# Kernel optimization log

Hardware: AMD Instinct MI355X
Metric: run time of the kernel (lower is better)

Reference implementation:

```python
import jax, jax.numpy as jnp
import numpy as np

G = 8           # graphs
NBG = 1024      # blocks per graph
APB = 4         # atoms per block
NC = 1          # coord channels
HID = 512
ES = 64
K = 9
L = 3
NLVL = 50
NB = G * NBG
NU = NB * APB
NUM_BLOCK, NUM_ATOM, NUM_POS = 25, 16, 16
BIG = 1e9


def _cumsum_ids(seg_lengths, n):
    # faithful to torch: zeros, mark segment starts via cumsum(lengths)[:-1], cumsum
    ids = jnp.zeros((n,), jnp.int32).at[jnp.cumsum(seg_lengths)[:-1]].set(1)
    return jnp.cumsum(ids)


def setup_inputs() -> dict:
    key = jax.random.key(0)
    ks = jax.random.split(key, 18)
    s = 0.02
    return {
        'Z': 3.0 * jax.random.normal(ks[0], (NU, NC, 3), jnp.float32),
        'B': jax.random.randint(ks[1], (NB,), 0, NUM_BLOCK),
        'A': jax.random.randint(ks[2], (NU,), 0, NUM_ATOM),
        'atom_positions': jax.random.randint(ks[3], (NU,), 0, NUM_POS),
        'block_lengths': jnp.full((NB,), APB, jnp.int32),
        'lengths': jnp.full((G,), NBG, jnp.int32),
        'segment_ids': jax.random.randint(ks[4], (NB,), 0, 2),
        'noise': jax.random.normal(ks[5], (NU, NC, 3), jnp.float32),
        'noise_level': jax.random.randint(ks[6], (G,), 0, NLVL),
        'sigmas': jnp.asarray(np.exp(np.linspace(np.log(10.0), np.log(0.01), NLVL)), jnp.float32),
        'atom_emb': s * jax.random.normal(ks[7], (NUM_ATOM, HID), jnp.float32),
        'pos_emb': s * jax.random.normal(ks[8], (NUM_POS, HID), jnp.float32),
        'block_emb': s * jax.random.normal(ks[9], (NUM_BLOCK, HID), jnp.float32),
        'edge_emb': s * jax.random.normal(ks[10], (2, ES), jnp.float32),
        'Wm': s * jax.random.normal(ks[11], (L, HID, HID), jnp.float32),
        'We': s * jax.random.normal(ks[12], (L, ES, HID), jnp.float32),
        'Wu': s * jax.random.normal(ks[13], (L, HID, HID), jnp.float32),
        'wz': s * jax.random.normal(ks[14], (L, HID), jnp.float32),
        'W1': s * jax.random.normal(ks[15], (HID, HID), jnp.float32),
        'b1': jnp.zeros((HID,), jnp.float32),
        'W2': s * jax.random.normal(ks[16], (HID, 1), jnp.float32),
    }


def _forward(Z, B, A, atom_positions, block_lengths, lengths, segment_ids,
             noise, noise_level, sigmas, atom_emb, pos_emb, block_emb, edge_emb,
             Wm, We, Wu, wz, W1, b1, W2):
    nb, nu, g = B.shape[0], A.shape[0], lengths.shape[0]
    nbg, apb = nb // g, nu // nb
    batch_id = _cumsum_ids(lengths, nb)        # [Nb]
    block_id = _cumsum_ids(block_lengths, nu)  # [Nu]

    # perturb: Z + noise * sigma[noise_level[graph]]
    used = sigmas[noise_level][batch_id][block_id]          # [Nu]
    Zp = Z + noise * used[:, None, None]                    # [Nu, NC, 3]

    # block embedding: atom + position + block-type
    H0 = atom_emb[A] + pos_emb[atom_positions] + block_emb[B][block_id]  # [Nu, H]

    # edges: fully connect -> split intra/inter by segment -> knn by min atom-pair distance
    xa = Zp.reshape(g, nbg * apb * NC, 3)
    sq = jnp.sum(xa * xa, axis=-1)
    d2 = sq[:, :, None] + sq[:, None, :] - 2.0 * jnp.einsum('gnd,gmd->gnm', xa, xa)
    D = d2.reshape(g, nbg, apb * NC, nbg, apb * NC).min(axis=(2, 4))     # [g, nbg, nbg]
    seg = segment_ids.reshape(g, nbg)
    same = seg[:, :, None] == seg[:, None, :]
    eye = jnp.eye(nbg, dtype=bool)[None]
    _, idx_intra = jax.lax.top_k(-jnp.where(same & ~eye, D, BIG), K)     # [g, nbg, K]
    _, idx_inter = jax.lax.top_k(-jnp.where(~same, D, BIG), K)
    off = (jnp.arange(g, dtype=jnp.int32) * nbg)[:, None, None]
    dst_loc = jnp.broadcast_to(jnp.arange(nbg, dtype=jnp.int32)[None, :, None] + off, (g, nbg, K))
    src = jnp.concatenate([(idx_intra + off).reshape(-1), (idx_inter + off).reshape(-1)])
    dst = jnp.concatenate([dst_loc.reshape(-1), dst_loc.reshape(-1)])
    eattr = edge_emb[jnp.concatenate([jnp.zeros(g * nbg * K, jnp.int32), jnp.ones(g * nbg * K, jnp.int32)])]

    # encoder (GET surrogate): block-level equivariant message passing
    h = jax.ops.segment_sum(H0, block_id, num_segments=nb) / apb                    # [Nb, H]
    Zb0 = jax.ops.segment_sum(Zp.mean(axis=1), block_id, num_segments=nb) / apb    # [Nb, 3]
    Zb = Zb0
    for l in range(Wm.shape[0]):
        m = jax.nn.silu((h[src] + h[dst]) @ Wm[l] + eattr @ We[l])                  # [E, H]
        h = h + jax.nn.silu(jax.ops.segment_sum(m, dst, num_segments=nb) @ Wu[l])
        coef = jnp.tanh(m @ wz[l])                                                  # [E]
        Zb = Zb + jax.ops.segment_sum((Zb[src] - Zb[dst]) * coef[:, None], dst, num_segments=nb) / (2 * K)
    pred_Z = Zp + (Zb - Zb0)[block_id][:, None, :]
    unit_repr = H0 + h[block_id]
    block_repr = h
    graph_repr = jax.ops.segment_sum(h, batch_id, num_segments=g)

    # energy head: SiLU -> Linear -> SiLU -> Linear(no bias), summed per graph
    e = jax.nn.silu(jax.nn.silu(block_repr) @ W1 + b1) @ W2                         # [Nb, 1]
    pred_energy = jax.ops.segment_sum(e[:, 0], batch_id, num_segments=g)            # [g]

    pred_noise = pred_Z - Zp
    per_unit = jnp.sum((pred_noise - noise) ** 2, axis=(-1, -2))                    # [Nu]
    nl = jax.ops.segment_sum(per_unit, batch_id[block_id], num_segments=g)
    loss = 0.5 * nl.mean()
    return pred_energy, pred_noise, unit_repr, block_repr, graph_repr, loss


def reference(Z, B, A, atom_positions, block_lengths, lengths, segment_ids,
              noise, noise_level, sigmas, atom_emb, pos_emb, block_emb, edge_emb,
              Wm, We, Wu, wz, W1, b1, W2):
    return _forward(Z, B, A, atom_positions, block_lengths, lengths, segment_ids,
                    noise, noise_level, sigmas, atom_emb, pos_emb, block_emb, edge_emb,
                    Wm, We, Wu, wz, W1, b1, W2)
```

## Files before the change

### kernel.cpp

```cpp
#include <hip/hip_runtime.h>
#include <hip/hip_bf16.h>

typedef __bf16 bf16;
typedef __bf16 bf16x2 __attribute__((ext_vector_type(2)));
typedef __bf16 bf16x8 __attribute__((ext_vector_type(8)));
typedef float floatx4 __attribute__((ext_vector_type(4)));

#define NB_ 8192
#define NU_ 32768

__device__ __forceinline__ float silu_f(float x) {
    float e = __expf(-x);
    return x * __builtin_amdgcn_rcpf(1.0f + e);
}

__global__ void transpose_weights(const float* __restrict__ Wm, const float* __restrict__ Wu,
                                  const float* __restrict__ W1,
                                  bf16* __restrict__ WmT, bf16* __restrict__ WuT, bf16* __restrict__ W1T) {
    int z = blockIdx.z;
    const float* src; bf16* dst;
    if (z < 3)      { src = Wm + (size_t)z*262144;     dst = WmT + (size_t)z*262144; }
    else if (z < 6) { src = Wu + (size_t)(z-3)*262144; dst = WuT + (size_t)(z-3)*262144; }
    else            { src = W1;                        dst = W1T; }
    __shared__ float tile[32][33];
    int tx = threadIdx.x, ty = threadIdx.y;
    int x = blockIdx.x*32 + tx;
    int y0 = blockIdx.y*32;
    #pragma unroll
    for (int i = 0; i < 32; i += 8)
        tile[ty+i][tx] = src[(size_t)(y0+ty+i)*512 + x];
    __syncthreads();
    int xo = blockIdx.y*32 + tx;
    int yo0 = blockIdx.x*32;
    #pragma unroll
    for (int i = 0; i < 32; i += 8)
        dst[(size_t)(yo0+ty+i)*512 + xo] = (bf16)tile[tx][ty+i];
}

__global__ void ebias_kernel(const float* __restrict__ edge_emb, const float* __restrict__ We,
                             float* __restrict__ ebias) {
    int gid = blockIdx.x*256 + threadIdx.x;
    if (gid >= 3072) return;
    int l = gid >> 10, t = (gid >> 9) & 1, c = gid & 511;
    float s = 0.0f;
    #pragma unroll 8
    for (int e = 0; e < 64; e++)
        s += edge_emb[t*64 + e] * We[(size_t)(l*64 + e)*512 + c];
    ebias[gid] = s;
}

__global__ void setup_kernel(const float* __restrict__ Z, const float* __restrict__ noise,
                             const int* __restrict__ noise_level, const float* __restrict__ sigmas,
                             const int* __restrict__ Aarr, const int* __restrict__ posa,
                             const int* __restrict__ Barr,
                             const float* __restrict__ atom_emb, const float* __restrict__ pos_emb,
                             const float* __restrict__ block_emb,
                             float* __restrict__ Zp, float* __restrict__ Zb0, float* __restrict__ Zb,
                             float* __restrict__ hf, bf16* __restrict__ hb) {
    int b = blockIdx.x;
    int tid = threadIdx.x;
    int g = b >> 10;
    __shared__ float zsh[12];
    if (tid < 12) {
        float sig = sigmas[noise_level[g]];
        int idx = b*12 + tid;
        float zp = Z[idx] + noise[idx]*sig;
        Zp[idx] = zp;
        zsh[tid] = zp;
    }
    __syncthreads();
    if (tid < 3) {
        float v = 0.25f*(zsh[tid] + zsh[3+tid] + zsh[6+tid] + zsh[9+tid]);
        Zb0[b*3+tid] = v; Zb[b*3+tid] = v;
    }
    int ai[4], pi[4];
    #pragma unroll
    for (int a = 0; a < 4; a++) { ai[a] = Aarr[b*4+a]*512; pi[a] = posa[b*4+a]*512; }
    int bb = Barr[b]*512;
    for (int c = tid; c < 512; c += 128) {
        float s = 0.0f;
        #pragma unroll
        for (int a = 0; a < 4; a++) s += atom_emb[ai[a]+c] + pos_emb[pi[a]+c];
        s = 0.25f*s + block_emb[bb+c];
        hf[(size_t)b*512+c] = s;
        hb[(size_t)b*512+c] = (bf16)s;
    }
}

__global__ __launch_bounds__(256) void knn_kernel(const float* __restrict__ Zp,
                                                  const int* __restrict__ seg,
                                                  int* __restrict__ nbr) {
    int wid = threadIdx.x >> 6;
    int lane = threadIdx.x & 63;
    int r = blockIdx.x*4 + wid;
    int g = r >> 10;
    int il = r & 1023;
    int segr = seg[r];
    float za[4][3];
    #pragma unroll
    for (int a = 0; a < 4; a++)
        #pragma unroll
        for (int d = 0; d < 3; d++)
            za[a][d] = Zp[r*12 + a*3 + d];
    float dist[16];
    unsigned smask = 0;
    int base = g << 10;
    #pragma unroll
    for (int t = 0; t < 16; t++) {
        int j = t*64 + lane;
        int jb = base + j;
        const float4* p = (const float4*)(Zp + (size_t)jb*12);
        float4 v0 = p[0], v1 = p[1], v2 = p[2];
        float bx[4] = {v0.x, v0.w, v1.z, v2.y};
        float by[4] = {v0.y, v1.x, v1.w, v2.z};
        float bz[4] = {v0.z, v1.y, v2.x, v2.w};
        float dm = 3.0e38f;
        #pragma unroll
        for (int a = 0; a < 4; a++) {
            #pragma unroll
            for (int bq = 0; bq < 4; bq++) {
                float dx = za[a][0]-bx[bq], dy = za[a][1]-by[bq], dz = za[a][2]-bz[bq];
                float dd = dx*dx + dy*dy + dz*dz;
                dm = fminf(dm, dd);
            }
        }
        dist[t] = dm;
        if (seg[jb] == segr) smask |= (1u << t);
    }
    unsigned removed = 0;
    for (int phase = 0; phase < 2; phase++) {
        for (int it = 0; it < 9; it++) {
            float bestd = 3.0e38f; int bestt = 0;
            #pragma unroll
            for (int t = 0; t < 16; t++) {
                int j = t*64 + lane;
                bool ok = (phase == 0) ? (((smask>>t)&1u) && (j != il))
                                       : (!((smask>>t)&1u));
                ok = ok && !((removed>>t)&1u);
                float dv = ok ? dist[t] : 1.0e9f;
                if (dv < bestd) { bestd = dv; bestt = t; }
            }
            int bestj = bestt*64 + lane;
            unsigned long long key =
                (((unsigned long long)__float_as_uint(bestd)) << 32) | (unsigned)bestj;
            #pragma unroll
            for (int off = 32; off >= 1; off >>= 1) {
                unsigned long long o = __shfl_xor(key, off, 64);
                if (o < key) key = o;
            }
            int jwin = (int)(key & 0xffffffffu);
            if (lane == 0) nbr[r*18 + phase*9 + it] = base + jwin;
            if ((jwin & 63) == lane) removed |= (1u << (jwin >> 6));
        }
    }
}

__global__ __launch_bounds__(256) void gemm_kernel(const bf16* __restrict__ A, const bf16* __restrict__ BT,
                                                   float* __restrict__ C, float* __restrict__ hf,
                                                   bf16* __restrict__ hb, bf16* __restrict__ shp,
                                                   const float* __restrict__ b1,
                                                   const float* __restrict__ W2,
                                                   float* __restrict__ eblk,
                                                   int mode) {
    int bid = blockIdx.x;
    int mt = bid & 63, nt = bid >> 6;
    int m0 = mt*128, n0 = nt*64;
    int tid = threadIdx.x, lane = tid & 63, wid = tid >> 6;
    int wm = wid & 1, wn = wid >> 1;
    int lm = lane & 15, q = lane >> 4;
    __shared__ alignas(16) bf16 sA[128*40];
    __shared__ alignas(16) bf16 sB[64*40];
    floatx4 zv = {0.0f, 0.0f, 0.0f, 0.0f};
    floatx4 acc[4][2];
    #pragma unroll
    for (int i = 0; i < 4; i++)
        #pragma unroll
        for (int j = 0; j < 2; j++) acc[i][j] = zv;
    for (int k0 = 0; k0 < 512; k0 += 32) {
        #pragma unroll
        for (int it = 0; it < 2; it++) {
            int idx = tid + it*256;
            int row = idx >> 2, qt = idx & 3;
            *(int4*)(sA + row*40 + qt*8) = *(const int4*)(A + (size_t)(m0+row)*512 + k0 + qt*8);
        }
        {
            int row = tid >> 2, qt = tid & 3;
            *(int4*)(sB + row*40 + qt*8) = *(const int4*)(BT + (size_t)(n0+row)*512 + k0 + qt*8);
        }
        __syncthreads();
        bf16x8 af[4], bfr[2];
        #pragma unroll
        for (int tm = 0; tm < 4; tm++)
            af[tm] = *(const bf16x8*)(sA + (wm*64 + tm*16 + lm)*40 + q*8);
        #pragma unroll
        for (int tn = 0; tn < 2; tn++)
            bfr[tn] = *(const bf16x8*)(sB + (wn*32 + tn*16 + lm)*40 + q*8);
        #pragma unroll
        for (int tm = 0; tm < 4; tm++)
            #pragma unroll
            for (int tn = 0; tn < 2; tn++)
                acc[tm][tn] = __builtin_amdgcn_mfma_f32_16x16x32_bf16(af[tm], bfr[tn], acc[tm][tn], 0, 0, 0);
        __syncthreads();
    }
    if (mode == 2) {
        #pragma unroll
        for (int tm = 0; tm < 4; tm++) {
            #pragma unroll
            for (int rr = 0; rr < 4; rr++) {
                float part = 0.0f;
                #pragma unroll
                for (int tn = 0; tn < 2; tn++) {
                    int col = n0 + wn*32 + tn*16 + lm;
                    float t = silu_f(acc[tm][tn][rr] + b1[col]);
                    part += t * W2[col];
                }
                part += __shfl_xor(part, 1, 64);
                part += __shfl_xor(part, 2, 64);
                part += __shfl_xor(part, 4, 64);
                part += __shfl_xor(part, 8, 64);
                if (lm == 0) {
                    int row = m0 + wm*64 + tm*16 + q*4 + rr;
                    atomicAdd(&eblk[row], part);
                }
            }
        }
        return;
    }
    #pragma unroll
    for (int tm = 0; tm < 4; tm++) {
        #pragma unroll
        for (int tn = 0; tn < 2; tn++) {
            #pragma unroll
            for (int rr = 0; rr < 4; rr++) {
                int row = m0 + wm*64 + tm*16 + q*4 + rr;
                int col = n0 + wn*32 + tn*16 + lm;
                size_t o = (size_t)row*512 + col;
                float v = acc[tm][tn][rr];
                if (mode == 0) {
                    C[o] = v;
                } else {
                    float nh = hf[o] + silu_f(v);
                    hf[o] = nh;
                    hb[o] = (bf16)nh;
                    if (shp) shp[o] = (bf16)silu_f(nh);
                }
            }
        }
    }
}

__global__ __launch_bounds__(256) void edge_kernel(const float* __restrict__ P, const float* __restrict__ ebias,
                                                   const float* __restrict__ wz, const float* __restrict__ Zb,
                                                   const int* __restrict__ nbr, bf16* __restrict__ msum,
                                                   float* __restrict__ zacc) {
    int b = blockIdx.x, tid = threadIdx.x;
    int c0 = 2*tid;
    int lane = tid & 63, wid = tid >> 6;
    __shared__ int srcs[18];
    __shared__ float red[18][4];
    __shared__ float term[18][3];
    if (tid < 18) srcs[tid] = nbr[b*18 + tid];
    __syncthreads();
    float2 pd  = *(const float2*)(P + (size_t)b*512 + c0);
    float2 eb0 = *(const float2*)(ebias + c0);
    float2 eb1 = *(const float2*)(ebias + 512 + c0);
    float2 w   = *(const float2*)(wz + c0);
    float ms0 = 0.0f, ms1 = 0.0f;
    float pdot[18];
    #pragma unroll
    for (int e = 0; e < 18; e++) {
        int s = srcs[e];
        float2 pv = *(const float2*)(P + (size_t)s*512 + c0);
        float ba = (e < 9) ? eb0.x : eb1.x;
        float bb = (e < 9) ? eb0.y : eb1.y;
        float m0 = silu_f(pv.x + pd.x + ba);
        float m1 = silu_f(pv.y + pd.y + bb);
        ms0 += m0; ms1 += m1;
        pdot[e] = m0*w.x + m1*w.y;
    }
    bf16x2 mp = { (bf16)ms0, (bf16)ms1 };
    *(bf16x2*)(msum + (size_t)b*512 + c0) = mp;
    #pragma unroll
    for (int e = 0; e < 18; e++) {
        float v = pdot[e];
        #pragma unroll
        for (int off = 32; off >= 1; off >>= 1) v += __shfl_xor(v, off, 64);
        if (lane == 0) red[e][wid] = v;
    }
    __syncthreads();
    if (tid < 18) {
        float dot = red[tid][0] + red[tid][1] + red[tid][2] + red[tid][3];
        float coef = tanhf(dot);
        int s = srcs[tid];
        #pragma unroll
        for (int d = 0; d < 3; d++)
            term[tid][d] = (Zb[s*3 + d] - Zb[b*3 + d]) * coef;
    }
    __syncthreads();
    if (tid < 3) {
        float s = 0.0f;
        #pragma unroll
        for (int e = 0; e < 18; e++) s += term[e][tid];
        zacc[b*3 + tid] = s;
    }
}

__global__ void zb_apply(float* __restrict__ Zb, const float* __restrict__ zacc) {
    int i = blockIdx.x*256 + threadIdx.x;
    if (i < NB_*3) Zb[i] += zacc[i] * (1.0f/18.0f);
}

__global__ void energy_kernel(const float* __restrict__ eblk, float* __restrict__ out_e) {
    int g = blockIdx.x, tid = threadIdx.x;
    __shared__ float red[256];
    float s = 0.0f;
    #pragma unroll
    for (int k = 0; k < 4; k++) s += eblk[g*1024 + k*256 + tid];
    red[tid] = s; __syncthreads();
    for (int st = 128; st > 0; st >>= 1) {
        if (tid < st) red[tid] += red[tid+st];
        __syncthreads();
    }
    if (tid == 0) out_e[g] = red[0];
}

__global__ void graphrepr_kernel(const float* __restrict__ h, float* __restrict__ out_gr) {
    int g = blockIdx.x >> 5;
    int rc = (blockIdx.x >> 1) & 15;
    int ch = blockIdx.x & 1;
    int c = ch*256 + threadIdx.x;
    int b0 = (g << 10) + rc*64;
    float s = 0.0f;
    for (int i = 0; i < 64; i++) s += h[(size_t)(b0+i)*512 + c];
    atomicAdd(&out_gr[g*512 + c], s);
}

__global__ void prednoise_loss_kernel(const float* __restrict__ Zb, const float* __restrict__ Zb0,
                                      const float* __restrict__ noise,
                                      float* __restrict__ out_pn, float* __restrict__ out_loss) {
    int u = blockIdx.x*256 + threadIdx.x;
    int b = u >> 2;
    float per = 0.0f;
    #pragma unroll
    for (int d = 0; d < 3; d++) {
        float dv = Zb[b*3+d] - Zb0[b*3+d];
        out_pn[u*3+d] = dv;
        float e = dv - noise[u*3+d];
        per += e*e;
    }
    __shared__ float red[256];
    red[threadIdx.x] = per; __syncthreads();
    for (int st = 128; st > 0; st >>= 1) {
        if (threadIdx.x < st) red[threadIdx.x] += red[threadIdx.x+st];
        __syncthreads();
    }
    if (threadIdx.x == 0) atomicAdd(out_loss, red[0] * (1.0f/16.0f));
}

__global__ void unitrepr_kernel(const int* __restrict__ Aarr, const int* __restrict__ posa,
                                const int* __restrict__ Barr,
                                const float* __restrict__ atom_emb, const float* __restrict__ pos_emb,
                                const float* __restrict__ block_emb,
                                const float* __restrict__ h, float* __restrict__ out_ur) {
    #pragma unroll
    for (int k = 0; k < 4; k++) {
        int idx = blockIdx.x*1024 + k*256 + threadIdx.x;
        int u = idx >> 9, c = idx & 511, b = u >> 2;
        out_ur[idx] = atom_emb[Aarr[u]*512+c] + pos_emb[posa[u]*512+c]
                    + block_emb[Barr[b]*512+c] + h[(size_t)b*512+c];
    }
}

extern "C" void kernel_launch(void* const* d_in, const int* in_sizes, int n_in,
                              void* d_out, int out_size, void* d_ws, size_t ws_size,
                              hipStream_t stream) {
    const float* Z         = (const float*)d_in[0];
    const int*   B         = (const int*)d_in[1];
    const int*   A         = (const int*)d_in[2];
    const int*   ap        = (const int*)d_in[3];
    const int*   seg       = (const int*)d_in[6];
    const float* noise     = (const float*)d_in[7];
    const int*   nl        = (const int*)d_in[8];
    const float* sig       = (const float*)d_in[9];
    const float* atom_emb  = (const float*)d_in[10];
    const float* pos_emb   = (const float*)d_in[11];
    const float* block_emb = (const float*)d_in[12];
    const float* edge_emb  = (const float*)d_in[13];
    const float* Wm        = (const float*)d_in[14];
    const float* We        = (const float*)d_in[15];
    const float* Wu        = (const float*)d_in[16];
    const float* wz        = (const float*)d_in[17];
    const float* W1        = (const float*)d_in[18];
    const float* b1        = (const float*)d_in[19];
    const float* W2        = (const float*)d_in[20];
    (void)in_sizes; (void)n_in; (void)d_ws; (void)ws_size; (void)out_size;

    float* out = (float*)d_out;
    const size_t o1 = 8, o2 = 98312, o3 = 16875528, o4 = 21069832, o5 = 21073928;
    float* out_e    = out;
    float* out_pn   = out + o1;
    float* out_ur   = out + o2;
    float* hf       = out + o3;
    float* out_gr   = out + o4;
    float* out_loss = out + o5;

    char* arena = (char*)(out + o2);
    float* P    = (float*)(arena);
    bf16*  msum = (bf16*)(arena + 16777216);
    bf16*  sh   = (bf16*)(arena + 25165824);
    bf16*  hb   = (bf16*)(arena + 33554432);
    float* Zp   = (float*)(arena + 41943040);
    float* Zb0  = (float*)(arena + 42336256);
    float* Zb   = (float*)(arena + 42434560);
    float* zacc = (float*)(arena + 42532864);
    int*   nbr  = (int*)  (arena + 42631168);
    bf16*  WmT  = (bf16*) (arena + 43220992);
    bf16*  WuT  = (bf16*) (arena + 44793856);
    bf16*  W1T  = (bf16*) (arena + 46366720);
    float* ebias= (float*)(arena + 46891008);
    float* eblk = (float*)(arena + 46903296);

    hipMemsetAsync(out_loss, 0, 4, stream);
    hipMemsetAsync(out_gr, 0, 8*512*4, stream);
    hipMemsetAsync(eblk, 0, NB_*4, stream);
    transpose_weights<<<dim3(16,16,7), dim3(32,8), 0, stream>>>(Wm, Wu, W1, WmT, WuT, W1T);
    ebias_kernel<<<12, 256, 0, stream>>>(edge_emb, We, ebias);
    setup_kernel<<<8192, 128, 0, stream>>>(Z, noise, nl, sig, A, ap, B,
                                           atom_emb, pos_emb, block_emb,
                                           Zp, Zb0, Zb, hf, hb);
    knn_kernel<<<2048, 256, 0, stream>>>(Zp, seg, nbr);
    for (int l = 0; l < 3; l++) {
        gemm_kernel<<<512, 256, 0, stream>>>(hb, WmT + (size_t)l*262144, P,
                                             nullptr, nullptr, nullptr, nullptr, nullptr, nullptr, 0);
        edge_kernel<<<8192, 256, 0, stream>>>(P, ebias + l*1024, wz + l*512, Zb, nbr, msum, zacc);
        gemm_kernel<<<512, 256, 0, stream>>>(msum, WuT + (size_t)l*262144, nullptr,
                                             hf, hb, (l == 2) ? sh : nullptr, nullptr, nullptr, nullptr, 1);
        zb_apply<<<96, 256, 0, stream>>>(Zb, zacc);
    }
    gemm_kernel<<<512, 256, 0, stream>>>(sh, W1T, nullptr, nullptr, nullptr, nullptr,
                                         b1, W2, eblk, 2);
    energy_kernel<<<8, 256, 0, stream>>>(eblk, out_e);
    graphrepr_kernel<<<256, 256, 0, stream>>>(hf, out_gr);
    prednoise_loss_kernel<<<128, 256, 0, stream>>>(Zb, Zb0, noise, out_pn, out_loss);
    unitrepr_kernel<<<16384, 256, 0, stream>>>(A, ap, B, atom_emb, pos_emb, block_emb, hf, out_ur);
}
```

Before: 528.9 us.

## Fuse setup kernels, overlap KNN with first GEMM, use bf16 P and LDS-direct loads

The init kernels (setup, weight transpose, ebias, memsets) are merged into one launch, and the KNN search is merged with the first message GEMM so the two run concurrently. zb_apply is folded into the update GEMM, and the energy, graph-repr and loss kernels are merged into one finalize kernel. The GEMM now uses global_load_lds with an XOR-swizzled LDS layout, the P intermediate is stored as bf16 to halve its traffic, KNN selection uses a float min-reduce plus ballot, and unitrepr is vectorised with float4. Risks: storing P in bf16 lowers precision, and the zb update inside the GEMM must not race with the edge kernel that reads Zb.

```diff
diff --git a/kernel.cpp b/kernel.cpp
--- a/kernel.cpp
+++ b/kernel.cpp
@@ -14,87 +14,109 @@
     return x * __builtin_amdgcn_rcpf(1.0f + e);
 }
 
-__global__ void transpose_weights(const float* __restrict__ Wm, const float* __restrict__ Wu,
-                                  const float* __restrict__ W1,
-                                  bf16* __restrict__ WmT, bf16* __restrict__ WuT, bf16* __restrict__ W1T) {
-    int z = blockIdx.z;
-    const float* src; bf16* dst;
-    if (z < 3)      { src = Wm + (size_t)z*262144;     dst = WmT + (size_t)z*262144; }
-    else if (z < 6) { src = Wu + (size_t)(z-3)*262144; dst = WuT + (size_t)(z-3)*262144; }
-    else            { src = W1;                        dst = W1T; }
+__device__ __forceinline__ float2 unpack_bf2(unsigned v) {
+    float2 r;
+    r.x = __uint_as_float(v << 16);
+    r.y = __uint_as_float(v & 0xFFFF0000u);
+    return r;
+}
+
+__device__ __forceinline__ void gll16(const bf16* g, bf16* l) {
+    __builtin_amdgcn_global_load_lds((const __attribute__((address_space(1))) void*)g,
+                                     (__attribute__((address_space(3))) void*)l, 16, 0, 0);
+}
+
+__global__ __launch_bounds__(256) void init_kernel(
+    const float* __restrict__ Z, const float* __restrict__ noise,
+    const int* __restrict__ nl, const float* __restrict__ sig,
+    const int* __restrict__ Aarr, const int* __restrict__ posa, const int* __restrict__ Barr,
+    const float* __restrict__ atom_emb, const float* __restrict__ pos_emb,
+    const float* __restrict__ block_emb,
+    const float* __restrict__ edge_emb, const float* __restrict__ We,
+    const float* __restrict__ Wm, const float* __restrict__ Wu, const float* __restrict__ W1,
+    float* __restrict__ Zp, float* __restrict__ Zb0, float* __restrict__ Zb,
+    float* __restrict__ hf, bf16* __restrict__ hb,
+    bf16* __restrict__ WmT, bf16* __restrict__ WuT, bf16* __restrict__ W1T,
+    float* __restrict__ ebias,
+    float* __restrict__ out_gr, float* __restrict__ eblk, float* __restrict__ out_loss)
+{
+    __shared__ float zsh[12];
     __shared__ float tile[32][33];
-    int tx = threadIdx.x, ty = threadIdx.y;
-    int x = blockIdx.x*32 + tx;
-    int y0 = blockIdx.y*32;
-    #pragma unroll
-    for (int i = 0; i < 32; i += 8)
-        tile[ty+i][tx] = src[(size_t)(y0+ty+i)*512 + x];
-    __syncthreads();
-    int xo = blockIdx.y*32 + tx;
-    int yo0 = blockIdx.x*32;
-    #pragma unroll
-    for (int i = 0; i < 32; i += 8)
-        dst[(size_t)(yo0+ty+i)*512 + xo] = (bf16)tile[tx][ty+i];
-}
-
-__global__ void ebias_kernel(const float* __restrict__ edge_emb, const float* __restrict__ We,
-                             float* __restrict__ ebias) {
-    int gid = blockIdx.x*256 + threadIdx.x;
-    if (gid >= 3072) return;
-    int l = gid >> 10, t = (gid >> 9) & 1, c = gid & 511;
-    float s = 0.0f;
-    #pragma unroll 8
-    for (int e = 0; e < 64; e++)
-        s += edge_emb[t*64 + e] * We[(size_t)(l*64 + e)*512 + c];
-    ebias[gid] = s;
-}
-
-__global__ void setup_kernel(const float* __restrict__ Z, const float* __restrict__ noise,
-                             const int* __restrict__ noise_level, const float* __restrict__ sigmas,
-                             const int* __restrict__ Aarr, const int* __restrict__ posa,
-                             const int* __restrict__ Barr,
-                             const float* __restrict__ atom_emb, const float* __restrict__ pos_emb,
-                             const float* __restrict__ block_emb,
-                             float* __restrict__ Zp, float* __restrict__ Zb0, float* __restrict__ Zb,
-                             float* __restrict__ hf, bf16* __restrict__ hb) {
-    int b = blockIdx.x;
-    int tid = threadIdx.x;
-    int g = b >> 10;
-    __shared__ float zsh[12];
-    if (tid < 12) {
-        float sig = sigmas[noise_level[g]];
-        int idx = b*12 + tid;
-        float zp = Z[idx] + noise[idx]*sig;
-        Zp[idx] = zp;
-        zsh[tid] = zp;
-    }
-    __syncthreads();
-    if (tid < 3) {
-        float v = 0.25f*(zsh[tid] + zsh[3+tid] + zsh[6+tid] + zsh[9+tid]);
-        Zb0[b*3+tid] = v; Zb[b*3+tid] = v;
-    }
-    int ai[4], pi[4];
-    #pragma unroll
-    for (int a = 0; a < 4; a++) { ai[a] = Aarr[b*4+a]*512; pi[a] = posa[b*4+a]*512; }
-    int bb = Barr[b]*512;
-    for (int c = tid; c < 512; c += 128) {
+    int bid = blockIdx.x, tid = threadIdx.x;
+    if (bid < 8192) {
+        int b = bid, g = b >> 10;
+        if (tid < 12) {
+            float sg = sig[nl[g]];
+            int idx = b*12 + tid;
+            float zp = Z[idx] + noise[idx]*sg;
+            Zp[idx] = zp;
+            zsh[tid] = zp;
+        }
+        __syncthreads();
+        if (tid < 3) {
+            float v = 0.25f*(zsh[tid] + zsh[3+tid] + zsh[6+tid] + zsh[9+tid]);
+            Zb0[b*3+tid] = v; Zb[b*3+tid] = v;
+        }
+        int ai[4], pi[4];
+        #pragma unroll
+        for (int a = 0; a < 4; a++) { ai[a] = Aarr[b*4+a]*512; pi[a] = posa[b*4+a]*512; }
+        int bb = Barr[b]*512;
+        #pragma unroll
+        for (int cc = 0; cc < 2; cc++) {
+            int c = tid + cc*256;
+            float s = 0.0f;
+            #pragma unroll
+            for (int a = 0; a < 4; a++) s += atom_emb[ai[a]+c] + pos_emb[pi[a]+c];
+            s = 0.25f*s + block_emb[bb+c];
+            hf[(size_t)b*512+c] = s;
+            hb[(size_t)b*512+c] = (bf16)s;
+        }
+        return;
+    }
+    bid -= 8192;
+    if (bid < 1792) {
+        int z = bid >> 8, rem = bid & 255;
+        int bx = rem & 15, by = rem >> 4;
+        int tx = tid & 31, ty = tid >> 5;
+        const float* src; bf16* dst;
+        if (z < 3)      { src = Wm + (size_t)z*262144;     dst = WmT + (size_t)z*262144; }
+        else if (z < 6) { src = Wu + (size_t)(z-3)*262144; dst = WuT + (size_t)(z-3)*262144; }
+        else            { src = W1;                        dst = W1T; }
+        #pragma unroll
+        for (int i = 0; i < 32; i += 8)
+            tile[ty+i][tx] = src[(size_t)(by*32+ty+i)*512 + bx*32+tx];
+        __syncthreads();
+        #pragma unroll
+        for (int i = 0; i < 32; i += 8)
+            dst[(size_t)(bx*32+ty+i)*512 + by*32+tx] = (bf16)tile[tx][ty+i];
+        return;
+    }
+    bid -= 1792;
+    if (bid < 12) {
+        int gid = bid*256 + tid;
+        int l = gid >> 10, t = (gid >> 9) & 1, c = gid & 511;
         float s = 0.0f;
-        #pragma unroll
-        for (int a = 0; a < 4; a++) s += atom_emb[ai[a]+c] + pos_emb[pi[a]+c];
-        s = 0.25f*s + block_emb[bb+c];
-        hf[(size_t)b*512+c] = s;
-        hb[(size_t)b*512+c] = (bf16)s;
-    }
-}
-
-__global__ __launch_bounds__(256) void knn_kernel(const float* __restrict__ Zp,
-                                                  const int* __restrict__ seg,
-                                                  int* __restrict__ nbr) {
+        #pragma unroll 8
+        for (int e = 0; e < 64; e++)
+            s += edge_emb[t*64 + e] * We[(size_t)(l*64 + e)*512 + c];
+        ebias[gid] = s;
+        return;
+    }
+    bid -= 12;
+    int k = bid*256 + tid;
+    if (k < 4096) out_gr[k] = 0.0f;
+    else if (k < 12288) eblk[k-4096] = 0.0f;
+    else if (k == 12288) out_loss[0] = 0.0f;
+}
+
+__device__ void knn_body(int kb, const float* __restrict__ Zp, const int* __restrict__ seg,
+                         int* __restrict__ nbr) {
     int wid = threadIdx.x >> 6;
     int lane = threadIdx.x & 63;
-    int r = blockIdx.x*4 + wid;
+    int r = ((kb & 7) << 10) + ((kb >> 3) << 2) + wid;
     int g = r >> 10;
     int il = r & 1023;
+    int base = g << 10;
     int segr = seg[r];
     float za[4][3];
     #pragma unroll
@@ -104,11 +126,9 @@
             za[a][d] = Zp[r*12 + a*3 + d];
     float dist[16];
     unsigned smask = 0;
-    int base = g << 10;
     #pragma unroll
     for (int t = 0; t < 16; t++) {
-        int j = t*64 + lane;
-        int jb = base + j;
+        int jb = base + t*64 + lane;
         const float4* p = (const float4*)(Zp + (size_t)jb*12);
         float4 v0 = p[0], v1 = p[1], v2 = p[2];
         float bx[4] = {v0.x, v0.w, v1.z, v2.y};
@@ -120,81 +140,90 @@
             #pragma unroll
             for (int bq = 0; bq < 4; bq++) {
                 float dx = za[a][0]-bx[bq], dy = za[a][1]-by[bq], dz = za[a][2]-bz[bq];
-                float dd = dx*dx + dy*dy + dz*dz;
-                dm = fminf(dm, dd);
+                dm = fminf(dm, dx*dx + dy*dy + dz*dz);
             }
         }
         dist[t] = dm;
         if (seg[jb] == segr) smask |= (1u << t);
     }
-    unsigned removed = 0;
+    const float INF = 3.0e38f;
     for (int phase = 0; phase < 2; phase++) {
+        float wd[16];
+        #pragma unroll
+        for (int t = 0; t < 16; t++) {
+            bool ok = (phase == 0) ? (((smask >> t) & 1u) && (t*64 + lane != il))
+                                   : (!((smask >> t) & 1u));
+            wd[t] = ok ? dist[t] : INF;
+        }
         for (int it = 0; it < 9; it++) {
-            float bestd = 3.0e38f; int bestt = 0;
-            #pragma unroll
-            for (int t = 0; t < 16; t++) {
-                int j = t*64 + lane;
-                bool ok = (phase == 0) ? (((smask>>t)&1u) && (j != il))
-                                       : (!((smask>>t)&1u));
-                ok = ok && !((removed>>t)&1u);
-                float dv = ok ? dist[t] : 1.0e9f;
-                if (dv < bestd) { bestd = dv; bestt = t; }
-            }
-            int bestj = bestt*64 + lane;
-            unsigned long long key =
-                (((unsigned long long)__float_as_uint(bestd)) << 32) | (unsigned)bestj;
-            #pragma unroll
-            for (int off = 32; off >= 1; off >>= 1) {
-                unsigned long long o = __shfl_xor(key, off, 64);
-                if (o < key) key = o;
-            }
-            int jwin = (int)(key & 0xffffffffu);
-            if (lane == 0) nbr[r*18 + phase*9 + it] = base + jwin;
-            if ((jwin & 63) == lane) removed |= (1u << (jwin >> 6));
-        }
-    }
-}
-
-__global__ __launch_bounds__(256) void gemm_kernel(const bf16* __restrict__ A, const bf16* __restrict__ BT,
-                                                   float* __restrict__ C, float* __restrict__ hf,
-                                                   bf16* __restrict__ hb, bf16* __restrict__ shp,
-                                                   const float* __restrict__ b1,
-                                                   const float* __restrict__ W2,
-                                                   float* __restrict__ eblk,
-                                                   int mode) {
-    int bid = blockIdx.x;
+            float bd = wd[0]; int bt = 0;
+            #pragma unroll
+            for (int t = 1; t < 16; t++) { if (wd[t] < bd) { bd = wd[t]; bt = t; } }
+            float mv = bd;
+            #pragma unroll
+            for (int off = 32; off >= 1; off >>= 1) mv = fminf(mv, __shfl_xor(mv, off, 64));
+            unsigned long long msk = __ballot(bd == mv);
+            int wl = __ffsll(msk) - 1;
+            int wt = __shfl(bt, wl, 64);
+            if (lane == 0) nbr[r*18 + phase*9 + it] = base + wt*64 + wl;
+            bool amwin = (lane == wl);
+            #pragma unroll
+            for (int t = 0; t < 16; t++) if (amwin && t == wt) wd[t] = INF;
+        }
+    }
+}
+
+__device__ void gemm_body(const bf16* __restrict__ A, const bf16* __restrict__ BT,
+                          bf16* __restrict__ Pb, float* __restrict__ hf,
+                          bf16* __restrict__ hb, bf16* __restrict__ shp,
+                          const float* __restrict__ b1, const float* __restrict__ W2,
+                          float* __restrict__ eblk,
+                          float* __restrict__ Zb, const float* __restrict__ zacc,
+                          int mode, int bid)
+{
+    __shared__ alignas(16) bf16 sA[128*32];
+    __shared__ alignas(16) bf16 sB[64*32];
     int mt = bid & 63, nt = bid >> 6;
     int m0 = mt*128, n0 = nt*64;
-    int tid = threadIdx.x, lane = tid & 63, wid = tid >> 6;
-    int wm = wid & 1, wn = wid >> 1;
+    int tid = threadIdx.x, lane = tid & 63, w = tid >> 6;
+    int wm = w & 1, wn = w >> 1;
     int lm = lane & 15, q = lane >> 4;
-    __shared__ alignas(16) bf16 sA[128*40];
-    __shared__ alignas(16) bf16 sB[64*40];
+
+    int pA0 = w*128 + lane, pA1 = pA0 + 64, pB = w*64 + lane;
+    int rA0 = pA0 >> 2, qA0 = (pA0 & 3) ^ ((rA0 >> 1) & 3);
+    int rA1 = pA1 >> 2, qA1 = (pA1 & 3) ^ ((rA1 >> 1) & 3);
+    int rB  = pB  >> 2, qB  = (pB  & 3) ^ ((rB  >> 1) & 3);
+    const bf16* gA0 = A  + (size_t)(m0 + rA0)*512 + qA0*8;
+    const bf16* gA1 = A  + (size_t)(m0 + rA1)*512 + qA1*8;
+    const bf16* gB  = BT + (size_t)(n0 + rB )*512 + qB*8;
+    bf16* lA0 = sA + (w*128)*8;
+    bf16* lA1 = sA + (w*128 + 64)*8;
+    bf16* lB  = sB + (w*64)*8;
+
+    int swq = (q ^ ((lm >> 1) & 3)) * 8;
+    const bf16* pa[4]; const bf16* pb2[2];
+    #pragma unroll
+    for (int tm = 0; tm < 4; tm++) pa[tm] = sA + (wm*64 + tm*16 + lm)*32 + swq;
+    #pragma unroll
+    for (int tn = 0; tn < 2; tn++) pb2[tn] = sB + (wn*32 + tn*16 + lm)*32 + swq;
+
     floatx4 zv = {0.0f, 0.0f, 0.0f, 0.0f};
     floatx4 acc[4][2];
     #pragma unroll
     for (int i = 0; i < 4; i++)
         #pragma unroll
         for (int j = 0; j < 2; j++) acc[i][j] = zv;
+
     for (int k0 = 0; k0 < 512; k0 += 32) {
-        #pragma unroll
-        for (int it = 0; it < 2; it++) {
-            int idx = tid + it*256;
-            int row = idx >> 2, qt = idx & 3;
-            *(int4*)(sA + row*40 + qt*8) = *(const int4*)(A + (size_t)(m0+row)*512 + k0 + qt*8);
-        }
-        {
-            int row = tid >> 2, qt = tid & 3;
-            *(int4*)(sB + row*40 + qt*8) = *(const int4*)(BT + (size_t)(n0+row)*512 + k0 + qt*8);
-        }
+        gll16(gA0 + k0, lA0);
+        gll16(gA1 + k0, lA1);
+        gll16(gB  + k0, lB);
         __syncthreads();
         bf16x8 af[4], bfr[2];
         #pragma unroll
-        for (int tm = 0; tm < 4; tm++)
-            af[tm] = *(const bf16x8*)(sA + (wm*64 + tm*16 + lm)*40 + q*8);
-        #pragma unroll
-        for (int tn = 0; tn < 2; tn++)
-            bfr[tn] = *(const bf16x8*)(sB + (wn*32 + tn*16 + lm)*40 + q*8);
+        for (int tm = 0; tm < 4; tm++) af[tm] = *(const bf16x8*)pa[tm];
+        #pragma unroll
+        for (int tn = 0; tn < 2; tn++) bfr[tn] = *(const bf16x8*)pb2[tn];
         #pragma unroll
         for (int tm = 0; tm < 4; tm++)
             #pragma unroll
@@ -202,6 +231,16 @@
                 acc[tm][tn] = __builtin_amdgcn_mfma_f32_16x16x32_bf16(af[tm], bfr[tn], acc[tm][tn], 0, 0, 0);
         __syncthreads();
     }
+
+    if (mode == 1 && nt == 0) {
+        int o = m0*3 + tid;
+        Zb[o] += zacc[o] * (1.0f/18.0f);
+        if (tid < 128) {
+            int o2 = m0*3 + 256 + tid;
+            Zb[o2] += zacc[o2] * (1.0f/18.0f);
+        }
+    }
+
     if (mode == 2) {
         #pragma unroll
         for (int tm = 0; tm < 4; tm++) {
@@ -237,7 +276,7 @@
                 size_t o = (size_t)row*512 + col;
                 float v = acc[tm][tn][rr];
                 if (mode == 0) {
-                    C[o] = v;
+                    Pb[o] = (bf16)v;
                 } else {
                     float nh = hf[o] + silu_f(v);
                     hf[o] = nh;
@@ -249,11 +288,35 @@
     }
 }
 
-__global__ __launch_bounds__(256) void edge_kernel(const float* __restrict__ P, const float* __restrict__ ebias,
+__global__ __launch_bounds__(256) void gemm_kernel(const bf16* __restrict__ A, const bf16* __restrict__ BT,
+                                                   bf16* __restrict__ Pb, float* __restrict__ hf,
+                                                   bf16* __restrict__ hb, bf16* __restrict__ shp,
+                                                   const float* __restrict__ b1, const float* __restrict__ W2,
+                                                   float* __restrict__ eblk,
+                                                   float* __restrict__ Zb, const float* __restrict__ zacc,
+                                                   int mode) {
+    gemm_body(A, BT, Pb, hf, hb, shp, b1, W2, eblk, Zb, zacc, mode, blockIdx.x);
+}
+
+__global__ __launch_bounds__(256) void knn_pgemm0_kernel(const bf16* __restrict__ hb,
+                                                         const bf16* __restrict__ WmT0,
+                                                         bf16* __restrict__ Pb,
+                                                         const float* __restrict__ Zp,
+                                                         const int* __restrict__ seg,
+                                                         int* __restrict__ nbr) {
+    if (blockIdx.x < 512)
+        gemm_body(hb, WmT0, Pb, nullptr, nullptr, nullptr, nullptr, nullptr, nullptr,
+                  nullptr, nullptr, 0, blockIdx.x);
+    else
+        knn_body(blockIdx.x - 512, Zp, seg, nbr);
+}
+
+__global__ __launch_bounds__(256) void edge_kernel(const bf16* __restrict__ Pb, const float* __restrict__ ebias,
                                                    const float* __restrict__ wz, const float* __restrict__ Zb,
                                                    const int* __restrict__ nbr, bf16* __restrict__ msum,
                                                    float* __restrict__ zacc) {
-    int b = blockIdx.x, tid = threadIdx.x;
+    int bid = blockIdx.x, tid = threadIdx.x;
+    int b = ((bid & 7) << 10) | (bid >> 3);
     int c0 = 2*tid;
     int lane = tid & 63, wid = tid >> 6;
     __shared__ int srcs[18];
@@ -261,7 +324,7 @@
     __shared__ float term[18][3];
     if (tid < 18) srcs[tid] = nbr[b*18 + tid];
     __syncthreads();
-    float2 pd  = *(const float2*)(P + (size_t)b*512 + c0);
+    float2 pd  = unpack_bf2(*(const unsigned*)(Pb + (size_t)b*512 + c0));
     float2 eb0 = *(const float2*)(ebias + c0);
     float2 eb1 = *(const float2*)(ebias + 512 + c0);
     float2 w   = *(const float2*)(wz + c0);
@@ -270,7 +333,7 @@
     #pragma unroll
     for (int e = 0; e < 18; e++) {
         int s = srcs[e];
-        float2 pv = *(const float2*)(P + (size_t)s*512 + c0);
+        float2 pv = unpack_bf2(*(const unsigned*)(Pb + (size_t)s*512 + c0));
         float ba = (e < 9) ? eb0.x : eb1.x;
         float bb = (e < 9) ? eb0.y : eb1.y;
         float m0 = silu_f(pv.x + pd.x + ba);
@@ -305,70 +368,73 @@
     }
 }
 
-__global__ void zb_apply(float* __restrict__ Zb, const float* __restrict__ zacc) {
-    int i = blockIdx.x*256 + threadIdx.x;
-    if (i < NB_*3) Zb[i] += zacc[i] * (1.0f/18.0f);
-}
-
-__global__ void energy_kernel(const float* __restrict__ eblk, float* __restrict__ out_e) {
-    int g = blockIdx.x, tid = threadIdx.x;
+__global__ __launch_bounds__(256) void finalize_kernel(const float* __restrict__ eblk, float* __restrict__ out_e,
+                                                       const float* __restrict__ hf, float* __restrict__ out_gr,
+                                                       const float* __restrict__ Zb, const float* __restrict__ Zb0,
+                                                       const float* __restrict__ noise,
+                                                       float* __restrict__ out_pn, float* __restrict__ out_loss) {
     __shared__ float red[256];
-    float s = 0.0f;
-    #pragma unroll
-    for (int k = 0; k < 4; k++) s += eblk[g*1024 + k*256 + tid];
-    red[tid] = s; __syncthreads();
-    for (int st = 128; st > 0; st >>= 1) {
-        if (tid < st) red[tid] += red[tid+st];
-        __syncthreads();
-    }
-    if (tid == 0) out_e[g] = red[0];
-}
-
-__global__ void graphrepr_kernel(const float* __restrict__ h, float* __restrict__ out_gr) {
-    int g = blockIdx.x >> 5;
-    int rc = (blockIdx.x >> 1) & 15;
-    int ch = blockIdx.x & 1;
-    int c = ch*256 + threadIdx.x;
+    int bid = blockIdx.x, tid = threadIdx.x;
+    if (bid < 8) {
+        int g = bid;
+        float s = 0.0f;
+        #pragma unroll
+        for (int k = 0; k < 4; k++) s += eblk[g*1024 + k*256 + tid];
+        red[tid] = s; __syncthreads();
+        for (int st = 128; st > 0; st >>= 1) {
+            if (tid < st) red[tid] += red[tid+st];
+            __syncthreads();
+        }
+        if (tid == 0) out_e[g] = red[0];
+        return;
+    }
+    if (bid < 136) {
+        int u = (bid-8)*256 + tid;
+        int b = u >> 2;
+        float per = 0.0f;
+        #pragma unroll
+        for (int d = 0; d < 3; d++) {
+            float dv = Zb[b*3+d] - Zb0[b*3+d];
+            out_pn[u*3+d] = dv;
+            float e = dv - noise[u*3+d];
+            per += e*e;
+        }
+        red[tid] = per; __syncthreads();
+        for (int st = 128; st > 0; st >>= 1) {
+            if (tid < st) red[tid] += red[tid+st];
+            __syncthreads();
+        }
+        if (tid == 0) atomicAdd(out_loss, red[0] * (1.0f/16.0f));
+        return;
+    }
+    int pid = bid - 136;
+    int g = pid >> 5;
+    int rc = (pid >> 1) & 15;
+    int ch = pid & 1;
+    int c = ch*256 + tid;
     int b0 = (g << 10) + rc*64;
     float s = 0.0f;
-    for (int i = 0; i < 64; i++) s += h[(size_t)(b0+i)*512 + c];
+    for (int i = 0; i < 64; i++) s += hf[(size_t)(b0+i)*512 + c];
     atomicAdd(&out_gr[g*512 + c], s);
 }
 
-__global__ void prednoise_loss_kernel(const float* __restrict__ Zb, const float* __restrict__ Zb0,
-                                      const float* __restrict__ noise,
-                                      float* __restrict__ out_pn, float* __restrict__ out_loss) {
-    int u = blockIdx.x*256 + threadIdx.x;
-    int b = u >> 2;
-    float per = 0.0f;
-    #pragma unroll
-    for (int d = 0; d < 3; d++) {
-        float dv = Zb[b*3+d] - Zb0[b*3+d];
-        out_pn[u*3+d] = dv;
-        float e = dv - noise[u*3+d];
-        per += e*e;
-    }
-    __shared__ float red[256];
-    red[threadIdx.x] = per; __syncthreads();
-    for (int st = 128; st > 0; st >>= 1) {
-        if (threadIdx.x < st) red[threadIdx.x] += red[threadIdx.x+st];
-        __syncthreads();
-    }
-    if (threadIdx.x == 0) atomicAdd(out_loss, red[0] * (1.0f/16.0f));
-}
-
-__global__ void unitrepr_kernel(const int* __restrict__ Aarr, const int* __restrict__ posa,
-                                const int* __restrict__ Barr,
-                                const float* __restrict__ atom_emb, const float* __restrict__ pos_emb,
-                                const float* __restrict__ block_emb,
-                                const float* __restrict__ h, float* __restrict__ out_ur) {
-    #pragma unroll
-    for (int k = 0; k < 4; k++) {
-        int idx = blockIdx.x*1024 + k*256 + threadIdx.x;
-        int u = idx >> 9, c = idx & 511, b = u >> 2;
-        out_ur[idx] = atom_emb[Aarr[u]*512+c] + pos_emb[posa[u]*512+c]
-                    + block_emb[Barr[b]*512+c] + h[(size_t)b*512+c];
-    }
+__global__ __launch_bounds__(256) void unitrepr_kernel(const int* __restrict__ Aarr, const int* __restrict__ posa,
+                                                       const int* __restrict__ Barr,
+                                                       const float* __restrict__ atom_emb, const float* __restrict__ pos_emb,
+                                                       const float* __restrict__ block_emb,
+                                                       const float* __restrict__ hf, float* __restrict__ out_ur) {
+    int gid = blockIdx.x*256 + threadIdx.x;
+    int u = gid >> 7, c = (gid & 127) << 2, b = u >> 2;
+    float4 va = *(const float4*)(atom_emb + (size_t)Aarr[u]*512 + c);
+    float4 vp = *(const float4*)(pos_emb + (size_t)posa[u]*512 + c);
+    float4 vb = *(const float4*)(block_emb + (size_t)Barr[b]*512 + c);
+    float4 vh = *(const float4*)(hf + (size_t)b*512 + c);
+    float4 o;
+    o.x = va.x + vp.x + vb.x + vh.x;
+    o.y = va.y + vp.y + vb.y + vh.y;
+    o.z = va.z + vp.z + vb.z + vh.z;
+    o.w = va.w + vp.w + vb.w + vh.w;
+    *(float4*)(out_ur + (size_t)u*512 + c) = o;
 }
 
 extern "C" void kernel_launch(void* const* d_in, const int* in_sizes, int n_in,
@@ -405,7 +471,7 @@
     float* out_loss = out + o5;
 
     char* arena = (char*)(out + o2);
-    float* P    = (float*)(arena);
+    bf16*  Pb   = (bf16*)(arena);
     bf16*  msum = (bf16*)(arena + 16777216);
     bf16*  sh   = (bf16*)(arena + 25165824);
     bf16*  hb   = (bf16*)(arena + 33554432);
@@ -420,27 +486,25 @@
     float* ebias= (float*)(arena + 46891008);
     float* eblk = (float*)(arena + 46903296);
 
-    hipMemsetAsync(out_loss, 0, 4, stream);
-    hipMemsetAsync(out_gr, 0, 8*512*4, stream);
-    hipMemsetAsync(eblk, 0, NB_*4, stream);
-    transpose_weights<<<dim3(16,16,7), dim3(32,8), 0, stream>>>(Wm, Wu, W1, WmT, WuT, W1T);
-    ebias_kernel<<<12, 256, 0, stream>>>(edge_emb, We, ebias);
-    setup_kernel<<<8192, 128, 0, stream>>>(Z, noise, nl, sig, A, ap, B,
-                                           atom_emb, pos_emb, block_emb,
-                                           Zp, Zb0, Zb, hf, hb);
-    knn_kernel<<<2048, 256, 0, stream>>>(Zp, seg, nbr);
+    init_kernel<<<8192 + 1792 + 12 + 49, 256, 0, stream>>>(
+        Z, noise, nl, sig, A, ap, B, atom_emb, pos_emb, block_emb,
+        edge_emb, We, Wm, Wu, W1,
+        Zp, Zb0, Zb, hf, hb, WmT, WuT, W1T, ebias, out_gr, eblk, out_loss);
+
+    knn_pgemm0_kernel<<<512 + 2048, 256, 0, stream>>>(hb, WmT, Pb, Zp, seg, nbr);
+
     for (int l = 0; l < 3; l++) {
-        gemm_kernel<<<512, 256, 0, stream>>>(hb, WmT + (size_t)l*262144, P,
-                                             nullptr, nullptr, nullptr, nullptr, nullptr, nullptr, 0);
-        edge_kernel<<<8192, 256, 0, stream>>>(P, ebias + l*1024, wz + l*512, Zb, nbr, msum, zacc);
+        if (l > 0)
+            gemm_kernel<<<512, 256, 0, stream>>>(hb, WmT + (size_t)l*262144, Pb,
+                                                 nullptr, nullptr, nullptr, nullptr, nullptr, nullptr,
+                                                 nullptr, nullptr, 0);
+        edge_kernel<<<8192, 256, 0, stream>>>(Pb, ebias + l*1024, wz + l*512, Zb, nbr, msum, zacc);
         gemm_kernel<<<512, 256, 0, stream>>>(msum, WuT + (size_t)l*262144, nullptr,
-                                             hf, hb, (l == 2) ? sh : nullptr, nullptr, nullptr, nullptr, 1);
-        zb_apply<<<96, 256, 0, stream>>>(Zb, zacc);
+                                             hf, hb, (l == 2) ? sh : nullptr, nullptr, nullptr, nullptr,
+                                             Zb, zacc, 1);
     }
     gemm_kernel<<<512, 256, 0, stream>>>(sh, W1T, nullptr, nullptr, nullptr, nullptr,
-                                         b1, W2, eblk, 2);
-    energy_kernel<<<8, 256, 0, stream>>>(eblk, out_e);
-    graphrepr_kernel<<<256, 256, 0, stream>>>(hf, out_gr);
-    prednoise_loss_kernel<<<128, 256, 0, stream>>>(Zb, Zb0, noise, out_pn, out_loss);
+                                         b1, W2, eblk, nullptr, nullptr, 2);
+    finalize_kernel<<<392, 256, 0, stream>>>(eblk, out_e, hf, out_gr, Zb, Zb0, noise, out_pn, out_loss);
     unitrepr_kernel<<<16384, 256, 0, stream>>>(A, ap, B, atom_emb, pos_emb, block_emb, hf, out_ur);
 }
```

Result: faster. 485.1 us (-8.3%).
